# Kernel tuning notes

Hardware: AMD Instinct MI355X
Metric: run time of the kernel (lower is better)

## Reference

```python
import jax, jax.numpy as jnp
import numpy as np

B, N, C, O, S = 32, 256, 512, 512, 512  # batch, table_num, in_ch, out_ch, s_dim


def setup_inputs() -> dict:
    key = jax.random.key(0)
    k1, k2, k3, k4 = jax.random.split(key, 4)
    # xavier_normal on (N, O, C): fan_in = O*C? torch treats dim0 fan_out, dim1 fan_in, rest receptive
    fan_out, fan_in = N * C, O * C
    std = float(np.sqrt(2.0 / (fan_in + fan_out)))
    weight = jax.random.normal(k1, (N, O, C), dtype=jnp.float32) * std
    bias = jnp.zeros((1, N, O), dtype=jnp.float32)
    # StyleGAN FullyConnectedLayer(s_dim -> table_num, bias_init=1): raw randn weight,
    # weight_gain = 1/sqrt(s_dim) applied at forward, bias init to 1
    s_w = jax.random.normal(k2, (N, S), dtype=jnp.float32)
    s_b = jnp.ones((N,), dtype=jnp.float32)
    x = jax.random.normal(k3, (B, N, C), dtype=jnp.float32)
    s = jax.random.normal(k4, (B, S), dtype=jnp.float32)
    return {"x": x, "s": s, "weight": weight, "bias": bias, "s_w": s_w, "s_b": s_b}


def reference(x, s, weight, bias, s_w, s_b):
    # style mapping: FullyConnectedLayer with weight_gain = 1/sqrt(s_dim)
    gain = 1.0 / np.sqrt(S)
    s_map = s @ (s_w.T * gain) + s_b  # (B, N)
    # demodulation: rsqrt(sum_c (weight*s)^2 + eps) == rsqrt(s^2 * sum_c weight^2 + eps)
    sumsq = jnp.sum(weight * weight, axis=-1)  # (N, O)
    decoefs = jax.lax.rsqrt(s_map[:, :, None] ** 2 * sumsq[None] + 1e-8)  # (B, N, O)
    xs = x * s_map[:, :, None]  # (B, N, C)
    out = jnp.einsum('noc,bnc->bno', weight, xs)  # (B, N, O)
    out = out * decoefs + bias
    return out
```

## Files before the change

kernel.cpp:

```cpp
#include <hip/hip_runtime.h>

#define B_ 32
#define N_ 256
#define C_ 512
#define O_ 512
#define S_ 512

typedef __attribute__((ext_vector_type(8))) short short8;
typedef __attribute__((ext_vector_type(4))) float f32x4;

__device__ __forceinline__ short f2bf(float f) {
    union { float f; unsigned u; } v; v.f = f;
    unsigned r = v.u + 0x7fffu + ((v.u >> 16) & 1u);
    return (short)(r >> 16);
}

__global__ __launch_bounds__(256) void tml_kernel(const float* __restrict__ x,
                                                  const float* __restrict__ s,
                                                  const float* __restrict__ weight,
                                                  const float* __restrict__ bias,
                                                  const float* __restrict__ s_w,
                                                  const float* __restrict__ s_b,
                                                  float* __restrict__ out) {
    const int h       = blockIdx.x;
    const int logical = (h & 7) * 128 + (h >> 3);
    const int n       = logical >> 2;
    const int ot      = logical & 3;

    const int tid  = threadIdx.x;
    const int wv   = tid >> 6;
    const int lane = tid & 63;
    const int l16  = lane & 15;
    const int lk   = lane >> 4;

    __shared__ short xs[B_][C_ + 8];
    __shared__ float sm_lds[B_];

    {
        const int b    = tid >> 3;
        const int slot = tid & 7;
        const float* sp = s   + (size_t)b * S_ + slot * 64;
        const float* wp = s_w + (size_t)n * S_ + slot * 64;
        float sum = 0.f;
#pragma unroll
        for (int j = 0; j < 16; ++j) {
            float4 sv = *(const float4*)(sp + 4 * j);
            float4 wv4 = *(const float4*)(wp + 4 * j);
            sum += sv.x * wv4.x + sv.y * wv4.y + sv.z * wv4.z + sv.w * wv4.w;
        }
        sum += __shfl_xor(sum, 1, 64);
        sum += __shfl_xor(sum, 2, 64);
        sum += __shfl_xor(sum, 4, 64);
        if (slot == 0) sm_lds[b] = sum * 0.04419417382415922f + s_b[n];
    }

    const float* xn = x + (size_t)n * C_;
#pragma unroll
    for (int r = 0; r < 16; ++r) {
        int i  = r * 256 + tid;
        int b  = i >> 7;
        int c4 = (i & 127) << 2;
        const float4 v = *(const float4*)(xn + (size_t)b * (N_ * C_) + c4);
        short4 hh;
        hh.x = f2bf(v.x); hh.y = f2bf(v.y); hh.z = f2bf(v.z); hh.w = f2bf(v.w);
        *(short4*)&xs[b][c4] = hh;
    }
    __syncthreads();

    const int ob = ot * 128 + wv * 32;
    const float* wrow = weight + (size_t)n * (O_ * C_) + (size_t)(ob + l16) * C_;

    f32x4 acc00 = {0.f,0.f,0.f,0.f}, acc01 = acc00, acc10 = acc00, acc11 = acc00;
    float ssq0 = 0.f, ssq1 = 0.f;

#pragma unroll 2
    for (int cb = 0; cb < C_; cb += 32) {
        const int co = cb + lk * 8;
        short8 a0 = *(const short8*)&xs[l16][co];
        short8 a1 = *(const short8*)&xs[16 + l16][co];
        float4 w00 = *(const float4*)(wrow + co);
        float4 w01 = *(const float4*)(wrow + co + 4);
        float4 w10 = *(const float4*)(wrow + 16 * C_ + co);
        float4 w11 = *(const float4*)(wrow + 16 * C_ + co + 4);

        ssq0 += w00.x*w00.x + w00.y*w00.y + w00.z*w00.z + w00.w*w00.w
              + w01.x*w01.x + w01.y*w01.y + w01.z*w01.z + w01.w*w01.w;
        ssq1 += w10.x*w10.x + w10.y*w10.y + w10.z*w10.z + w10.w*w10.w
              + w11.x*w11.x + w11.y*w11.y + w11.z*w11.z + w11.w*w11.w;

        short8 b0, b1;
        b0[0]=f2bf(w00.x); b0[1]=f2bf(w00.y); b0[2]=f2bf(w00.z); b0[3]=f2bf(w00.w);
        b0[4]=f2bf(w01.x); b0[5]=f2bf(w01.y); b0[6]=f2bf(w01.z); b0[7]=f2bf(w01.w);
        b1[0]=f2bf(w10.x); b1[1]=f2bf(w10.y); b1[2]=f2bf(w10.z); b1[3]=f2bf(w10.w);
        b1[4]=f2bf(w11.x); b1[5]=f2bf(w11.y); b1[6]=f2bf(w11.z); b1[7]=f2bf(w11.w);

        acc00 = __builtin_amdgcn_mfma_f32_16x16x32_bf16(a0, b0, acc00, 0, 0, 0);
        acc10 = __builtin_amdgcn_mfma_f32_16x16x32_bf16(a1, b0, acc10, 0, 0, 0);
        acc01 = __builtin_amdgcn_mfma_f32_16x16x32_bf16(a0, b1, acc01, 0, 0, 0);
        acc11 = __builtin_amdgcn_mfma_f32_16x16x32_bf16(a1, b1, acc11, 0, 0, 0);
    }

    ssq0 += __shfl_xor(ssq0, 16, 64);  ssq0 += __shfl_xor(ssq0, 32, 64);
    ssq1 += __shfl_xor(ssq1, 16, 64);  ssq1 += __shfl_xor(ssq1, 32, 64);

#pragma unroll
    for (int f = 0; f < 2; ++f) {
        const int o  = ob + f * 16 + l16;
        const float bv = bias[n * O_ + o];
        const float sq = f ? ssq1 : ssq0;
        const f32x4 am0 = f ? acc01 : acc00;
        const f32x4 am1 = f ? acc11 : acc10;
#pragma unroll
        for (int r = 0; r < 4; ++r) {
            {
                const int brow = lk * 4 + r;
                const float smv = sm_lds[brow];
                const float dec = rsqrtf(smv * smv * sq + 1e-8f);
                out[(size_t)brow * (N_ * O_) + n * O_ + o] = am0[r] * smv * dec + bv;
            }
            {
                const int brow = 16 + lk * 4 + r;
                const float smv = sm_lds[brow];
                const float dec = rsqrtf(smv * smv * sq + 1e-8f);
                out[(size_t)brow * (N_ * O_) + n * O_ + o] = am1[r] * smv * dec + bv;
            }
        }
    }
}

extern "C" void kernel_launch(void* const* d_in, const int* in_sizes, int n_in,
                              void* d_out, int out_size, void* d_ws, size_t ws_size,
                              hipStream_t stream) {
    const float* x      = (const float*)d_in[0];
    const float* s      = (const float*)d_in[1];
    const float* weight = (const float*)d_in[2];
    const float* bias   = (const float*)d_in[3];
    const float* s_w    = (const float*)d_in[4];
    const float* s_b    = (const float*)d_in[5];
    float* out = (float*)d_out;

    tml_kernel<<<N_ * 4, 256, 0, stream>>>(x, s, weight, bias, s_w, s_b, out);
}
```

Before: 66.30 us.

## Stage weight tiles through double-buffered LDS with register prefetch

Weight loads move from direct per-lane strided global reads to a cooperative coalesced load of 128x64 tiles. The tiles are converted to bf16 once and written into a double-buffered LDS tile, and the next tile is prefetched into registers while the current one is consumed by MFMA. The sum of squares is now computed from the bf16-rounded weights rather than fp32, which slightly changes numerics. It adds LDS usage and a barrier per k-tile, and sets launch_bounds occupancy hint to 2.

```diff
diff --git a/kernel.cpp b/kernel.cpp
--- a/kernel.cpp
+++ b/kernel.cpp
@@ -5,6 +5,10 @@
 #define C_ 512
 #define O_ 512
 #define S_ 512
+
+#define KT  64
+#define NKT (C_ / KT)
+#define WST 72
 
 typedef __attribute__((ext_vector_type(8))) short short8;
 typedef __attribute__((ext_vector_type(4))) float f32x4;
@@ -14,14 +18,18 @@
     unsigned r = v.u + 0x7fffu + ((v.u >> 16) & 1u);
     return (short)(r >> 16);
 }
+__device__ __forceinline__ float bf2f(short s) {
+    union { unsigned u; float f; } v; v.u = ((unsigned)(unsigned short)s) << 16;
+    return v.f;
+}
 
-__global__ __launch_bounds__(256) void tml_kernel(const float* __restrict__ x,
-                                                  const float* __restrict__ s,
-                                                  const float* __restrict__ weight,
-                                                  const float* __restrict__ bias,
-                                                  const float* __restrict__ s_w,
-                                                  const float* __restrict__ s_b,
-                                                  float* __restrict__ out) {
+__global__ __launch_bounds__(256, 2) void tml_kernel(const float* __restrict__ x,
+                                                     const float* __restrict__ s,
+                                                     const float* __restrict__ weight,
+                                                     const float* __restrict__ bias,
+                                                     const float* __restrict__ s_w,
+                                                     const float* __restrict__ s_b,
+                                                     float* __restrict__ out) {
     const int h       = blockIdx.x;
     const int logical = (h & 7) * 128 + (h >> 3);
     const int n       = logical >> 2;
@@ -34,7 +42,17 @@
     const int lk   = lane >> 4;
 
     __shared__ short xs[B_][C_ + 8];
+    __shared__ short wt[2][128][WST];
     __shared__ float sm_lds[B_];
+
+    const int srow = tid >> 4;
+    const int scol = tid & 15;
+    const float* wbase = weight + (size_t)n * (O_ * C_) + (size_t)(ot * 128) * C_ + scol * 4;
+
+    float4 rg0[8], rg1[8];
+#pragma unroll
+    for (int i = 0; i < 8; ++i)
+        rg0[i] = *(const float4*)(wbase + (size_t)(i * 16 + srow) * C_);
 
     {
         const int b    = tid >> 3;
@@ -44,7 +62,7 @@
         float sum = 0.f;
 #pragma unroll
         for (int j = 0; j < 16; ++j) {
-            float4 sv = *(const float4*)(sp + 4 * j);
+            float4 sv  = *(const float4*)(sp + 4 * j);
             float4 wv4 = *(const float4*)(wp + 4 * j);
             sum += sv.x * wv4.x + sv.y * wv4.y + sv.z * wv4.z + sv.w * wv4.w;
         }
@@ -65,44 +83,59 @@
         hh.x = f2bf(v.x); hh.y = f2bf(v.y); hh.z = f2bf(v.z); hh.w = f2bf(v.w);
         *(short4*)&xs[b][c4] = hh;
     }
-    __syncthreads();
-
-    const int ob = ot * 128 + wv * 32;
-    const float* wrow = weight + (size_t)n * (O_ * C_) + (size_t)(ob + l16) * C_;
 
     f32x4 acc00 = {0.f,0.f,0.f,0.f}, acc01 = acc00, acc10 = acc00, acc11 = acc00;
     float ssq0 = 0.f, ssq1 = 0.f;
 
-#pragma unroll 2
-    for (int cb = 0; cb < C_; cb += 32) {
-        const int co = cb + lk * 8;
-        short8 a0 = *(const short8*)&xs[l16][co];
-        short8 a1 = *(const short8*)&xs[16 + l16][co];
-        float4 w00 = *(const float4*)(wrow + co);
-        float4 w01 = *(const float4*)(wrow + co + 4);
-        float4 w10 = *(const float4*)(wrow + 16 * C_ + co);
-        float4 w11 = *(const float4*)(wrow + 16 * C_ + co + 4);
+#define STEP(T, RCUR, RNXT, PB)                                                   \
+    {                                                                             \
+        if ((T) + 1 < NKT) {                                                      \
+            _Pragma("unroll")                                                     \
+            for (int i = 0; i < 8; ++i)                                           \
+                RNXT[i] = *(const float4*)(wbase + (size_t)(i * 16 + srow) * C_   \
+                                           + ((T) + 1) * KT);                     \
+        }                                                                         \
+        _Pragma("unroll")                                                         \
+        for (int i = 0; i < 8; ++i) {                                             \
+            short4 hv;                                                            \
+            hv.x = f2bf(RCUR[i].x); hv.y = f2bf(RCUR[i].y);                       \
+            hv.z = f2bf(RCUR[i].z); hv.w = f2bf(RCUR[i].w);                       \
+            *(short4*)&wt[PB][i * 16 + srow][scol * 4] = hv;                      \
+        }                                                                         \
+        __syncthreads();                                                          \
+        _Pragma("unroll")                                                         \
+        for (int ks = 0; ks < KT / 32; ++ks) {                                    \
+            const int co = ks * 32 + lk * 8;                                      \
+            short8 a0 = *(const short8*)&xs[l16][(T) * KT + co];                  \
+            short8 a1 = *(const short8*)&xs[16 + l16][(T) * KT + co];             \
+            short8 b0 = *(const short8*)&wt[PB][wv * 32 + l16][co];               \
+            short8 b1 = *(const short8*)&wt[PB][wv * 32 + 16 + l16][co];          \
+            _Pragma("unroll")                                                     \
+            for (int j = 0; j < 8; ++j) {                                         \
+                float f0 = bf2f(b0[j]), f1 = bf2f(b1[j]);                         \
+                ssq0 += f0 * f0; ssq1 += f1 * f1;                                 \
+            }                                                                     \
+            acc00 = __builtin_amdgcn_mfma_f32_16x16x32_bf16(a0, b0, acc00, 0,0,0);\
+            acc10 = __builtin_amdgcn_mfma_f32_16x16x32_bf16(a1, b0, acc10, 0,0,0);\
+            acc01 = __builtin_amdgcn_mfma_f32_16x16x32_bf16(a0, b1, acc01, 0,0,0);\
+            acc11 = __builtin_amdgcn_mfma_f32_16x16x32_bf16(a1, b1, acc11, 0,0,0);\
+        }                                                                         \
+    }
 
-        ssq0 += w00.x*w00.x + w00.y*w00.y + w00.z*w00.z + w00.w*w00.w
-              + w01.x*w01.x + w01.y*w01.y + w01.z*w01.z + w01.w*w01.w;
-        ssq1 += w10.x*w10.x + w10.y*w10.y + w10.z*w10.z + w10.w*w10.w
-              + w11.x*w11.x + w11.y*w11.y + w11.z*w11.z + w11.w*w11.w;
-
-        short8 b0, b1;
-        b0[0]=f2bf(w00.x); b0[1]=f2bf(w00.y); b0[2]=f2bf(w00.z); b0[3]=f2bf(w00.w);
-        b0[4]=f2bf(w01.x); b0[5]=f2bf(w01.y); b0[6]=f2bf(w01.z); b0[7]=f2bf(w01.w);
-        b1[0]=f2bf(w10.x); b1[1]=f2bf(w10.y); b1[2]=f2bf(w10.z); b1[3]=f2bf(w10.w);
-        b1[4]=f2bf(w11.x); b1[5]=f2bf(w11.y); b1[6]=f2bf(w11.z); b1[7]=f2bf(w11.w);
-
-        acc00 = __builtin_amdgcn_mfma_f32_16x16x32_bf16(a0, b0, acc00, 0, 0, 0);
-        acc10 = __builtin_amdgcn_mfma_f32_16x16x32_bf16(a1, b0, acc10, 0, 0, 0);
-        acc01 = __builtin_amdgcn_mfma_f32_16x16x32_bf16(a0, b1, acc01, 0, 0, 0);
-        acc11 = __builtin_amdgcn_mfma_f32_16x16x32_bf16(a1, b1, acc11, 0, 0, 0);
-    }
+    STEP(0, rg0, rg1, 0)
+    STEP(1, rg1, rg0, 1)
+    STEP(2, rg0, rg1, 0)
+    STEP(3, rg1, rg0, 1)
+    STEP(4, rg0, rg1, 0)
+    STEP(5, rg1, rg0, 1)
+    STEP(6, rg0, rg1, 0)
+    STEP(7, rg1, rg0, 1)
+#undef STEP
 
     ssq0 += __shfl_xor(ssq0, 16, 64);  ssq0 += __shfl_xor(ssq0, 32, 64);
     ssq1 += __shfl_xor(ssq1, 16, 64);  ssq1 += __shfl_xor(ssq1, 32, 64);
 
+    const int ob = ot * 128 + wv * 32;
 #pragma unroll
     for (int f = 0; f < 2; ++f) {
         const int o  = ob + f * 16 + l16;
```

Result: faster. 63.16 us (-4.7%).

## Stage weight panel in LDS with register prefetch and split-K wave reduction

Applied to the files above, without the earlier changes.

Each block's 128-row weight panel is now streamed in 16-row chunks. Each chunk is prefetched into registers, converted to bf16 and written into a small LDS tile, while the previous chunk is consumed by MFMAs. The x operand is loaded straight into per-wave register A-fragments instead of a large LDS tile. K is split across wave pairs, and partial accumulators and sum-of-squares are reduced through LDS. The aim is to overlap the memory-bound weight stream with compute and raise occupancy, at the cost of extra barriers per chunk and computing the demodulation sum-of-squares from bf16-rounded weights.

```diff
diff --git a/kernel.cpp b/kernel.cpp
--- a/kernel.cpp
+++ b/kernel.cpp
@@ -5,6 +5,8 @@
 #define C_ 512
 #define O_ 512
 #define S_ 512
+
+#define WST 520
 
 typedef __attribute__((ext_vector_type(8))) short short8;
 typedef __attribute__((ext_vector_type(4))) float f32x4;
@@ -14,14 +16,18 @@
     unsigned r = v.u + 0x7fffu + ((v.u >> 16) & 1u);
     return (short)(r >> 16);
 }
+__device__ __forceinline__ float bf2f(short s) {
+    union { unsigned u; float f; } v; v.u = ((unsigned)(unsigned short)s) << 16;
+    return v.f;
+}
 
-__global__ __launch_bounds__(256) void tml_kernel(const float* __restrict__ x,
-                                                  const float* __restrict__ s,
-                                                  const float* __restrict__ weight,
-                                                  const float* __restrict__ bias,
-                                                  const float* __restrict__ s_w,
-                                                  const float* __restrict__ s_b,
-                                                  float* __restrict__ out) {
+__global__ __launch_bounds__(256, 4) void tml_kernel(const float* __restrict__ x,
+                                                     const float* __restrict__ s,
+                                                     const float* __restrict__ weight,
+                                                     const float* __restrict__ bias,
+                                                     const float* __restrict__ s_w,
+                                                     const float* __restrict__ s_b,
+                                                     float* __restrict__ out) {
     const int h       = blockIdx.x;
     const int logical = (h & 7) * 128 + (h >> 3);
     const int n       = logical >> 2;
@@ -29,12 +35,23 @@
 
     const int tid  = threadIdx.x;
     const int wv   = tid >> 6;
+    const int mb   = wv & 1;
+    const int kh   = wv >> 1;
     const int lane = tid & 63;
     const int l16  = lane & 15;
     const int lk   = lane >> 4;
 
-    __shared__ short xs[B_][C_ + 8];
+    __shared__ short wt[16][WST];
+    __shared__ f32x4 redv[2][64];
+    __shared__ float reds[2][64];
     __shared__ float sm_lds[B_];
+
+    const float* wpanel = weight + (size_t)n * (O_ * C_) + (size_t)(ot * 128) * C_;
+
+    float4 rg[8];
+#pragma unroll
+    for (int i = 0; i < 8; ++i)
+        rg[i] = *(const float4*)(wpanel + (size_t)(i * 256 + tid) * 4);
 
     {
         const int b    = tid >> 3;
@@ -44,7 +61,7 @@
         float sum = 0.f;
 #pragma unroll
         for (int j = 0; j < 16; ++j) {
-            float4 sv = *(const float4*)(sp + 4 * j);
+            float4 sv  = *(const float4*)(sp + 4 * j);
             float4 wv4 = *(const float4*)(wp + 4 * j);
             sum += sv.x * wv4.x + sv.y * wv4.y + sv.z * wv4.z + sv.w * wv4.w;
         }
@@ -54,77 +71,79 @@
         if (slot == 0) sm_lds[b] = sum * 0.04419417382415922f + s_b[n];
     }
 
-    const float* xn = x + (size_t)n * C_;
+    short8 afr[8];
+    {
+        const float* xb = x + ((size_t)(mb * 16 + l16) * N_ + n) * C_ + kh * 256 + lk * 8;
 #pragma unroll
-    for (int r = 0; r < 16; ++r) {
-        int i  = r * 256 + tid;
-        int b  = i >> 7;
-        int c4 = (i & 127) << 2;
-        const float4 v = *(const float4*)(xn + (size_t)b * (N_ * C_) + c4);
-        short4 hh;
-        hh.x = f2bf(v.x); hh.y = f2bf(v.y); hh.z = f2bf(v.z); hh.w = f2bf(v.w);
-        *(short4*)&xs[b][c4] = hh;
+        for (int ks = 0; ks < 8; ++ks) {
+            float4 u = *(const float4*)(xb + ks * 32);
+            float4 w = *(const float4*)(xb + ks * 32 + 4);
+            short8 a;
+            a[0] = f2bf(u.x); a[1] = f2bf(u.y); a[2] = f2bf(u.z); a[3] = f2bf(u.w);
+            a[4] = f2bf(w.x); a[5] = f2bf(w.y); a[6] = f2bf(w.z); a[7] = f2bf(w.w);
+            afr[ks] = a;
+        }
+    }
+
+#pragma unroll
+    for (int i = 0; i < 8; ++i) {
+        int f4 = i * 256 + tid;
+        int row = f4 >> 7, c4 = (f4 & 127) << 2;
+        short4 hv;
+        hv.x = f2bf(rg[i].x); hv.y = f2bf(rg[i].y); hv.z = f2bf(rg[i].z); hv.w = f2bf(rg[i].w);
+        *(short4*)&wt[row][c4] = hv;
     }
     __syncthreads();
 
-    const int ob = ot * 128 + wv * 32;
-    const float* wrow = weight + (size_t)n * (O_ * C_) + (size_t)(ob + l16) * C_;
+    for (int c = 0; c < 8; ++c) {
+        if (c + 1 < 8) {
+#pragma unroll
+            for (int i = 0; i < 8; ++i)
+                rg[i] = *(const float4*)(wpanel + (size_t)(c + 1) * 8192
+                                         + (size_t)(i * 256 + tid) * 4);
+        }
 
-    f32x4 acc00 = {0.f,0.f,0.f,0.f}, acc01 = acc00, acc10 = acc00, acc11 = acc00;
-    float ssq0 = 0.f, ssq1 = 0.f;
+        f32x4 acc = {0.f, 0.f, 0.f, 0.f};
+        float ssq = 0.f;
+#pragma unroll
+        for (int ks = 0; ks < 8; ++ks) {
+            short8 bf = *(const short8*)&wt[l16][kh * 256 + ks * 32 + lk * 8];
+#pragma unroll
+            for (int j = 0; j < 8; ++j) { float fv = bf2f(bf[j]); ssq += fv * fv; }
+            acc = __builtin_amdgcn_mfma_f32_16x16x32_bf16(afr[ks], bf, acc, 0, 0, 0);
+        }
+        ssq += __shfl_xor(ssq, 16, 64);
+        ssq += __shfl_xor(ssq, 32, 64);
 
-#pragma unroll 2
-    for (int cb = 0; cb < C_; cb += 32) {
-        const int co = cb + lk * 8;
-        short8 a0 = *(const short8*)&xs[l16][co];
-        short8 a1 = *(const short8*)&xs[16 + l16][co];
-        float4 w00 = *(const float4*)(wrow + co);
-        float4 w01 = *(const float4*)(wrow + co + 4);
-        float4 w10 = *(const float4*)(wrow + 16 * C_ + co);
-        float4 w11 = *(const float4*)(wrow + 16 * C_ + co + 4);
+        if (kh) { redv[mb][lane] = acc; reds[mb][lane] = ssq; }
+        __syncthreads();
 
-        ssq0 += w00.x*w00.x + w00.y*w00.y + w00.z*w00.z + w00.w*w00.w
-              + w01.x*w01.x + w01.y*w01.y + w01.z*w01.z + w01.w*w01.w;
-        ssq1 += w10.x*w10.x + w10.y*w10.y + w10.z*w10.z + w10.w*w10.w
-              + w11.x*w11.x + w11.y*w11.y + w11.z*w11.z + w11.w*w11.w;
-
-        short8 b0, b1;
-        b0[0]=f2bf(w00.x); b0[1]=f2bf(w00.y); b0[2]=f2bf(w00.z); b0[3]=f2bf(w00.w);
-        b0[4]=f2bf(w01.x); b0[5]=f2bf(w01.y); b0[6]=f2bf(w01.z); b0[7]=f2bf(w01.w);
-        b1[0]=f2bf(w10.x); b1[1]=f2bf(w10.y); b1[2]=f2bf(w10.z); b1[3]=f2bf(w10.w);
-        b1[4]=f2bf(w11.x); b1[5]=f2bf(w11.y); b1[6]=f2bf(w11.z); b1[7]=f2bf(w11.w);
-
-        acc00 = __builtin_amdgcn_mfma_f32_16x16x32_bf16(a0, b0, acc00, 0, 0, 0);
-        acc10 = __builtin_amdgcn_mfma_f32_16x16x32_bf16(a1, b0, acc10, 0, 0, 0);
-        acc01 = __builtin_amdgcn_mfma_f32_16x16x32_bf16(a0, b1, acc01, 0, 0, 0);
-        acc11 = __builtin_amdgcn_mfma_f32_16x16x32_bf16(a1, b1, acc11, 0, 0, 0);
-    }
-
-    ssq0 += __shfl_xor(ssq0, 16, 64);  ssq0 += __shfl_xor(ssq0, 32, 64);
-    ssq1 += __shfl_xor(ssq1, 16, 64);  ssq1 += __shfl_xor(ssq1, 32, 64);
-
+        if (c + 1 < 8) {
 #pragma unroll
-    for (int f = 0; f < 2; ++f) {
-        const int o  = ob + f * 16 + l16;
-        const float bv = bias[n * O_ + o];
-        const float sq = f ? ssq1 : ssq0;
-        const f32x4 am0 = f ? acc01 : acc00;
-        const f32x4 am1 = f ? acc11 : acc10;
-#pragma unroll
-        for (int r = 0; r < 4; ++r) {
-            {
-                const int brow = lk * 4 + r;
-                const float smv = sm_lds[brow];
-                const float dec = rsqrtf(smv * smv * sq + 1e-8f);
-                out[(size_t)brow * (N_ * O_) + n * O_ + o] = am0[r] * smv * dec + bv;
-            }
-            {
-                const int brow = 16 + lk * 4 + r;
-                const float smv = sm_lds[brow];
-                const float dec = rsqrtf(smv * smv * sq + 1e-8f);
-                out[(size_t)brow * (N_ * O_) + n * O_ + o] = am1[r] * smv * dec + bv;
+            for (int i = 0; i < 8; ++i) {
+                int f4 = i * 256 + tid;
+                int row = f4 >> 7, c4 = (f4 & 127) << 2;
+                short4 hv;
+                hv.x = f2bf(rg[i].x); hv.y = f2bf(rg[i].y);
+                hv.z = f2bf(rg[i].z); hv.w = f2bf(rg[i].w);
+                *(short4*)&wt[row][c4] = hv;
             }
         }
+        if (!kh) {
+            const f32x4 pacc = redv[mb][lane];
+            const float sq   = ssq + reds[mb][lane];
+            const int obase  = ot * 128 + c * 16;
+            const float bv   = bias[n * O_ + obase + l16];
+#pragma unroll
+            for (int r = 0; r < 4; ++r) {
+                const int b     = mb * 16 + lk * 4 + r;
+                const float smv = sm_lds[b];
+                const float dec = rsqrtf(smv * smv * sq + 1e-8f);
+                out[(size_t)b * (N_ * O_) + n * O_ + obase + l16] =
+                    (acc[r] + pacc[r]) * smv * dec + bv;
+            }
+        }
+        if (c + 1 < 8) __syncthreads();
     }
 }
 
```

Measured after the change: 73.62 us. +11.0%, slower.

## Stage weight tiles through double-buffered LDS with register prefetch, one block per table

Applied to the files above, without the earlier changes.

Each block now handles a whole table entry n (all 512 outputs) with 512 threads, instead of four blocks per n each handling 128 outputs. This stops the x tile and style vector from being recomputed four times. Weight K-tiles are loaded with coalesced row-major reads into registers one step ahead, converted to bf16 and written to a double-buffered LDS tile, then read by the waves as MFMA B operands. The sum of squares is now computed from the bf16-rounded weights, which slightly changes the demodulation precision. LDS use grows (about 114 KB per block) and each step needs a barrier, so occupancy and sync overhead may limit the gain.

```diff
diff --git a/kernel.cpp b/kernel.cpp
--- a/kernel.cpp
+++ b/kernel.cpp
@@ -5,6 +5,10 @@
 #define C_ 512
 #define O_ 512
 #define S_ 512
+
+#define KT  32
+#define NKT (C_ / KT)
+#define WST 40
 
 typedef __attribute__((ext_vector_type(8))) short short8;
 typedef __attribute__((ext_vector_type(4))) float f32x4;
@@ -14,19 +18,24 @@
     unsigned r = v.u + 0x7fffu + ((v.u >> 16) & 1u);
     return (short)(r >> 16);
 }
+__device__ __forceinline__ float bf2f(short s) {
+    union { unsigned u; float f; } v; v.u = ((unsigned)(unsigned short)s) << 16;
+    return v.f;
+}
 
-__global__ __launch_bounds__(256) void tml_kernel(const float* __restrict__ x,
-                                                  const float* __restrict__ s,
-                                                  const float* __restrict__ weight,
-                                                  const float* __restrict__ bias,
-                                                  const float* __restrict__ s_w,
-                                                  const float* __restrict__ s_b,
-                                                  float* __restrict__ out) {
-    const int h       = blockIdx.x;
-    const int logical = (h & 7) * 128 + (h >> 3);
-    const int n       = logical >> 2;
-    const int ot      = logical & 3;
+__device__ __forceinline__ void nd_barrier() {
+    asm volatile("s_waitcnt lgkmcnt(0)" ::: "memory");
+    __builtin_amdgcn_s_barrier();
+}
 
+__global__ __launch_bounds__(512, 2) void tml_kernel(const float* __restrict__ x,
+                                                     const float* __restrict__ s,
+                                                     const float* __restrict__ weight,
+                                                     const float* __restrict__ bias,
+                                                     const float* __restrict__ s_w,
+                                                     const float* __restrict__ s_b,
+                                                     float* __restrict__ out) {
+    const int n    = blockIdx.x;
     const int tid  = threadIdx.x;
     const int wv   = tid >> 6;
     const int lane = tid & 63;
@@ -34,30 +43,41 @@
     const int lk   = lane >> 4;
 
     __shared__ short xs[B_][C_ + 8];
+    __shared__ short wt[2][O_][WST];
     __shared__ float sm_lds[B_];
 
+    const int srow = tid >> 3;
+    const int scol = tid & 7;
+    const float* wbase = weight + (size_t)n * (O_ * C_) + scol * 4;
+
+    float4 rg0[8], rg1[8];
+#pragma unroll
+    for (int i = 0; i < 8; ++i)
+        rg0[i] = *(const float4*)(wbase + (size_t)(i * 64 + srow) * C_);
+
     {
-        const int b    = tid >> 3;
-        const int slot = tid & 7;
-        const float* sp = s   + (size_t)b * S_ + slot * 64;
-        const float* wp = s_w + (size_t)n * S_ + slot * 64;
+        const int b    = tid >> 4;
+        const int slot = tid & 15;
+        const float* sp = s   + (size_t)b * S_ + slot * 32;
+        const float* wp = s_w + (size_t)n * S_ + slot * 32;
         float sum = 0.f;
 #pragma unroll
-        for (int j = 0; j < 16; ++j) {
-            float4 sv = *(const float4*)(sp + 4 * j);
+        for (int j = 0; j < 8; ++j) {
+            float4 sv  = *(const float4*)(sp + 4 * j);
             float4 wv4 = *(const float4*)(wp + 4 * j);
             sum += sv.x * wv4.x + sv.y * wv4.y + sv.z * wv4.z + sv.w * wv4.w;
         }
         sum += __shfl_xor(sum, 1, 64);
         sum += __shfl_xor(sum, 2, 64);
         sum += __shfl_xor(sum, 4, 64);
+        sum += __shfl_xor(sum, 8, 64);
         if (slot == 0) sm_lds[b] = sum * 0.04419417382415922f + s_b[n];
     }
 
     const float* xn = x + (size_t)n * C_;
 #pragma unroll
-    for (int r = 0; r < 16; ++r) {
-        int i  = r * 256 + tid;
+    for (int r = 0; r < 8; ++r) {
+        int i  = r * 512 + tid;
         int b  = i >> 7;
         int c4 = (i & 127) << 2;
         const float4 v = *(const float4*)(xn + (size_t)b * (N_ * C_) + c4);
@@ -65,64 +85,87 @@
         hh.x = f2bf(v.x); hh.y = f2bf(v.y); hh.z = f2bf(v.z); hh.w = f2bf(v.w);
         *(short4*)&xs[b][c4] = hh;
     }
-    __syncthreads();
 
-    const int ob = ot * 128 + wv * 32;
-    const float* wrow = weight + (size_t)n * (O_ * C_) + (size_t)(ob + l16) * C_;
+    f32x4 acc[4][2];
+#pragma unroll
+    for (int f = 0; f < 4; ++f)
+#pragma unroll
+        for (int m = 0; m < 2; ++m) acc[f][m] = (f32x4){0.f, 0.f, 0.f, 0.f};
+    float ssq[4] = {0.f, 0.f, 0.f, 0.f};
 
-    f32x4 acc00 = {0.f,0.f,0.f,0.f}, acc01 = acc00, acc10 = acc00, acc11 = acc00;
-    float ssq0 = 0.f, ssq1 = 0.f;
-
-#pragma unroll 2
-    for (int cb = 0; cb < C_; cb += 32) {
-        const int co = cb + lk * 8;
-        short8 a0 = *(const short8*)&xs[l16][co];
-        short8 a1 = *(const short8*)&xs[16 + l16][co];
-        float4 w00 = *(const float4*)(wrow + co);
-        float4 w01 = *(const float4*)(wrow + co + 4);
-        float4 w10 = *(const float4*)(wrow + 16 * C_ + co);
-        float4 w11 = *(const float4*)(wrow + 16 * C_ + co + 4);
-
-        ssq0 += w00.x*w00.x + w00.y*w00.y + w00.z*w00.z + w00.w*w00.w
-              + w01.x*w01.x + w01.y*w01.y + w01.z*w01.z + w01.w*w01.w;
-        ssq1 += w10.x*w10.x + w10.y*w10.y + w10.z*w10.z + w10.w*w10.w
-              + w11.x*w11.x + w11.y*w11.y + w11.z*w11.z + w11.w*w11.w;
-
-        short8 b0, b1;
-        b0[0]=f2bf(w00.x); b0[1]=f2bf(w00.y); b0[2]=f2bf(w00.z); b0[3]=f2bf(w00.w);
-        b0[4]=f2bf(w01.x); b0[5]=f2bf(w01.y); b0[6]=f2bf(w01.z); b0[7]=f2bf(w01.w);
-        b1[0]=f2bf(w10.x); b1[1]=f2bf(w10.y); b1[2]=f2bf(w10.z); b1[3]=f2bf(w10.w);
-        b1[4]=f2bf(w11.x); b1[5]=f2bf(w11.y); b1[6]=f2bf(w11.z); b1[7]=f2bf(w11.w);
-
-        acc00 = __builtin_amdgcn_mfma_f32_16x16x32_bf16(a0, b0, acc00, 0, 0, 0);
-        acc10 = __builtin_amdgcn_mfma_f32_16x16x32_bf16(a1, b0, acc10, 0, 0, 0);
-        acc01 = __builtin_amdgcn_mfma_f32_16x16x32_bf16(a0, b1, acc01, 0, 0, 0);
-        acc11 = __builtin_amdgcn_mfma_f32_16x16x32_bf16(a1, b1, acc11, 0, 0, 0);
+#define STEP(T, RCUR, RNXT, PB)                                                     \
+    {                                                                               \
+        if ((T) + 1 < NKT) {                                                        \
+            _Pragma("unroll")                                                       \
+            for (int i = 0; i < 8; ++i)                                             \
+                RNXT[i] = *(const float4*)(wbase + (size_t)(i * 64 + srow) * C_     \
+                                           + ((T) + 1) * KT);                       \
+        }                                                                           \
+        _Pragma("unroll")                                                           \
+        for (int i = 0; i < 8; ++i) {                                               \
+            short4 hv;                                                              \
+            hv.x = f2bf(RCUR[i].x); hv.y = f2bf(RCUR[i].y);                         \
+            hv.z = f2bf(RCUR[i].z); hv.w = f2bf(RCUR[i].w);                         \
+            *(short4*)&wt[PB][i * 64 + srow][scol * 4] = hv;                        \
+        }                                                                           \
+        nd_barrier();                                                               \
+        {                                                                           \
+            const int co = lk * 8;                                                  \
+            short8 a0 = *(const short8*)&xs[l16][(T) * KT + co];                    \
+            short8 a1 = *(const short8*)&xs[16 + l16][(T) * KT + co];               \
+            _Pragma("unroll")                                                       \
+            for (int f = 0; f < 4; ++f) {                                           \
+                short8 bf = *(const short8*)&wt[PB][wv * 64 + f * 16 + l16][co];    \
+                _Pragma("unroll")                                                   \
+                for (int j = 0; j < 8; ++j) {                                       \
+                    float fv = bf2f(bf[j]); ssq[f] += fv * fv;                      \
+                }                                                                   \
+                acc[f][0] = __builtin_amdgcn_mfma_f32_16x16x32_bf16(a0, bf,         \
+                                                          acc[f][0], 0, 0, 0);     \
+                acc[f][1] = __builtin_amdgcn_mfma_f32_16x16x32_bf16(a1, bf,         \
+                                                          acc[f][1], 0, 0, 0);     \
+            }                                                                       \
+        }                                                                           \
     }
 
-    ssq0 += __shfl_xor(ssq0, 16, 64);  ssq0 += __shfl_xor(ssq0, 32, 64);
-    ssq1 += __shfl_xor(ssq1, 16, 64);  ssq1 += __shfl_xor(ssq1, 32, 64);
+    STEP(0,  rg0, rg1, 0)
+    STEP(1,  rg1, rg0, 1)
+    STEP(2,  rg0, rg1, 0)
+    STEP(3,  rg1, rg0, 1)
+    STEP(4,  rg0, rg1, 0)
+    STEP(5,  rg1, rg0, 1)
+    STEP(6,  rg0, rg1, 0)
+    STEP(7,  rg1, rg0, 1)
+    STEP(8,  rg0, rg1, 0)
+    STEP(9,  rg1, rg0, 1)
+    STEP(10, rg0, rg1, 0)
+    STEP(11, rg1, rg0, 1)
+    STEP(12, rg0, rg1, 0)
+    STEP(13, rg1, rg0, 1)
+    STEP(14, rg0, rg1, 0)
+    STEP(15, rg1, rg0, 1)
+#undef STEP
 
 #pragma unroll
-    for (int f = 0; f < 2; ++f) {
-        const int o  = ob + f * 16 + l16;
+    for (int f = 0; f < 4; ++f) {
+        ssq[f] += __shfl_xor(ssq[f], 16, 64);
+        ssq[f] += __shfl_xor(ssq[f], 32, 64);
+    }
+
+#pragma unroll
+    for (int f = 0; f < 4; ++f) {
+        const int o    = wv * 64 + f * 16 + l16;
         const float bv = bias[n * O_ + o];
-        const float sq = f ? ssq1 : ssq0;
-        const f32x4 am0 = f ? acc01 : acc00;
-        const f32x4 am1 = f ? acc11 : acc10;
+        const float sq = ssq[f];
 #pragma unroll
-        for (int r = 0; r < 4; ++r) {
-            {
-                const int brow = lk * 4 + r;
+        for (int m = 0; m < 2; ++m) {
+#pragma unroll
+            for (int r = 0; r < 4; ++r) {
+                const int brow  = m * 16 + lk * 4 + r;
                 const float smv = sm_lds[brow];
                 const float dec = rsqrtf(smv * smv * sq + 1e-8f);
-                out[(size_t)brow * (N_ * O_) + n * O_ + o] = am0[r] * smv * dec + bv;
-            }
-            {
-                const int brow = 16 + lk * 4 + r;
-                const float smv = sm_lds[brow];
-                const float dec = rsqrtf(smv * smv * sq + 1e-8f);
-                out[(size_t)brow * (N_ * O_) + n * O_ + o] = am1[r] * smv * dec + bv;
+                out[(size_t)brow * (N_ * O_) + n * O_ + o] =
+                    acc[f][m][r] * smv * dec + bv;
             }
         }
     }
@@ -139,5 +182,5 @@
     const float* s_b    = (const float*)d_in[5];
     float* out = (float*)d_out;
 
-    tml_kernel<<<N_ * 4, 256, 0, stream>>>(x, s, weight, bias, s_w, s_b, out);
+    tml_kernel<<<N_, 512, 0, stream>>>(x, s, weight, bias, s_w, s_b, out);
 }
```

After: 53.72 us. -19.0%, faster.
